# Kernel tuning notes

Hardware: AMD Instinct MI355X
Metric: run time of the kernel (lower is better)

Reference implementation:

```python
import jax, jax.numpy as jnp
import numpy as np

N_NODES = 10000
N_EDGES = 160000
HIDDEN = 64
NUM_RBF = 32
Q_DIM = 8
CUTOFF_UPPER = 5.0


def silu(x):
    return x * jax.nn.sigmoid(x)


def tensor_norm(X):
    # X: [n, 3, 3, H] -> [n, H] (Frobenius norm squared over the 3x3 dims)
    return (X * X).sum(axis=(1, 2))


def decompose_tensor(X):
    # X: [n, 3, 3, H] -> I: [n, H] (trace/3), A: antisym [n,3,3,H], S: sym traceless [n,3,3,H]
    eye = jnp.eye(3, dtype=X.dtype)[None, :, :, None]
    I = jnp.einsum('naah->nh', X) / 3.0
    Xt = X.transpose(0, 2, 1, 3)
    A = 0.5 * (X - Xt)
    S = 0.5 * (X + Xt) - I[:, None, None, :] * eye
    return I, A, S


def compose_tensor(I, A, S):
    eye = jnp.eye(3, dtype=A.dtype)[None, :, :, None]
    return I[:, None, None, :] * eye + A + S


def tmm(P, Q):
    # 3x3 matmul per (atom, channel): [n,3,3,H] x [n,3,3,H] -> [n,3,3,H]
    return jnp.einsum('nach,ncbh->nabh', P, Q)


def setup_inputs() -> dict:
    key = jax.random.key(0)
    ks = jax.random.split(key, 16)
    H = HIDDEN
    inp = {
        'X': jax.random.normal(ks[0], (N_NODES, 3, 3, H), jnp.float32),
        'charges': jax.random.normal(ks[1], (N_NODES, Q_DIM), jnp.float32),
        'edge_weight': jax.random.uniform(ks[2], (N_EDGES,), jnp.float32) * CUTOFF_UPPER,
        'edge_attr': jax.random.normal(ks[3], (N_EDGES, NUM_RBF), jnp.float32),
        'edge_index': jax.random.randint(ks[4], (2, N_EDGES), 0, N_NODES, jnp.int32),
    }
    d_in = NUM_RBF + 2 * Q_DIM
    inp['Ws1'] = jax.random.normal(ks[5], (d_in, H), jnp.float32) / np.sqrt(d_in).astype(np.float32)
    inp['bs1'] = jnp.zeros((H,), jnp.float32)
    inp['Ws2'] = jax.random.normal(ks[6], (H, 2 * H), jnp.float32) / np.sqrt(H).astype(np.float32)
    inp['bs2'] = jnp.zeros((2 * H,), jnp.float32)
    inp['Ws3'] = jax.random.normal(ks[7], (2 * H, 3 * H), jnp.float32) / np.sqrt(2 * H).astype(np.float32)
    inp['bs3'] = jnp.zeros((3 * H,), jnp.float32)
    for i in range(6):
        inp['Wt%d' % i] = jax.random.normal(ks[8 + i], (H, H), jnp.float32) / np.sqrt(H).astype(np.float32)
    return inp


def reference(X, charges, edge_weight, edge_attr, Ws1, bs1, Ws2, bs2, Ws3, bs3,
              Wt0, Wt1, Wt2, Wt3, Wt4, Wt5, edge_index):
    H = HIDDEN
    n = X.shape[0]
    row, col = edge_index[0], edge_index[1]
    # cosine cutoff (cutoff_lower = 0)
    C = 0.5 * (jnp.cos(edge_weight * (jnp.pi / CUTOFF_UPPER)) + 1.0)
    C = C * (edge_weight < CUTOFF_UPPER).astype(X.dtype)
    # edge scalar MLP on [rbf, q_i, q_j]
    h = jnp.concatenate([edge_attr, charges[row], charges[col]], axis=-1)
    h = silu(h @ Ws1 + bs1)
    h = silu(h @ Ws2 + bs2)
    h = silu(h @ Ws3 + bs3)
    w = (h * C[:, None]).reshape(h.shape[0], 3, H)  # [E, 3, H]
    # normalize node tensors
    X = X / (tensor_norm(X) + 1.0)[:, None, None, :]
    I, A, S = decompose_tensor(X)
    I = I @ Wt0
    A = A @ Wt1
    S = S @ Wt2
    Y = compose_tensor(I, A, S)
    # message passing: gather I/A/S at source (edge_index[1]), weight per component, scatter-add at dest (edge_index[0])
    eye = jnp.eye(3, dtype=X.dtype)[None, :, :, None]
    msg_e = ((w[:, 0] * I[col])[:, None, None, :] * eye
             + w[:, 1][:, None, None, :] * A[col]
             + w[:, 2][:, None, None, :] * S[col])  # [E, 3, 3, H]
    msg = jax.ops.segment_sum(msg_e, row, num_segments=n)  # [n, 3, 3, H]
    # O(3): C = msg @ Y + Y @ msg (3x3 matmul per channel)
    Cm = tmm(msg, Y) + tmm(Y, msg)
    I2, A2, S2 = decompose_tensor(Cm)
    normp1 = tensor_norm(Cm) + 1.0
    I2 = I2 / normp1
    A2 = A2 / normp1[:, None, None, :]
    S2 = S2 / normp1[:, None, None, :]
    I2 = I2 @ Wt3
    A2 = A2 @ Wt4
    S2 = S2 @ Wt5
    dX = compose_tensor(I2, A2, S2)
    return X + dX + tmm(dX, dX)
```

## Files before the change

### kernel.cpp

```cpp
#include <hip/hip_runtime.h>
#include <math.h>

#define HD 64

typedef _Float16 half8 __attribute__((ext_vector_type(8)));
typedef _Float16 half4v __attribute__((ext_vector_type(4)));
typedef float floatx4 __attribute__((ext_vector_type(4)));

__device__ __forceinline__ float silu_f(float x) {
    return x * __builtin_amdgcn_rcpf(1.0f + __expf(-x));
}

__global__ __launch_bounds__(256) void node_pre(
    const float* __restrict__ X,
    const float* __restrict__ Wt0, const float* __restrict__ Wt1, const float* __restrict__ Wt2,
    float* __restrict__ Tn, _Float16* __restrict__ TnH, int N)
{
    int sub = threadIdx.x >> 6;
    int h = threadIdx.x & 63;
    int n = blockIdx.x * 4 + sub;
    int nn = (n < N) ? n : (N - 1);

    const float* Xb = X + (size_t)nn * 9 * HD + h;
    float x[9];
    float nrm = 0.f;
#pragma unroll
    for (int i = 0; i < 9; ++i) { x[i] = Xb[i * HD]; nrm += x[i] * x[i]; }
    float inv = 1.0f / (nrm + 1.0f);
#pragma unroll
    for (int i = 0; i < 9; ++i) x[i] *= inv;

    float I0 = (x[0] + x[4] + x[8]) * (1.0f / 3.0f);
    __shared__ float comp[4][10][HD];
    comp[sub][0][h] = I0;
    comp[sub][1][h] = 0.5f * (x[1] - x[3]);
    comp[sub][2][h] = 0.5f * (x[2] - x[6]);
    comp[sub][3][h] = 0.5f * (x[5] - x[7]);
    comp[sub][4][h] = x[0] - I0;
    comp[sub][5][h] = 0.5f * (x[1] + x[3]);
    comp[sub][6][h] = 0.5f * (x[2] + x[6]);
    comp[sub][7][h] = x[4] - I0;
    comp[sub][8][h] = 0.5f * (x[5] + x[7]);
    comp[sub][9][h] = x[8] - I0;
    __syncthreads();
    float acc[10];
#pragma unroll
    for (int i = 0; i < 10; ++i) acc[i] = 0.f;
    for (int k = 0; k < HD; ++k) {
        float w0 = Wt0[k * HD + h];
        float w1 = Wt1[k * HD + h];
        float w2 = Wt2[k * HD + h];
        acc[0] += comp[sub][0][k] * w0;
        acc[1] += comp[sub][1][k] * w1;
        acc[2] += comp[sub][2][k] * w1;
        acc[3] += comp[sub][3][k] * w1;
#pragma unroll
        for (int j = 0; j < 6; ++j) acc[4 + j] += comp[sub][4 + j][k] * w2;
    }
    if (n < N) {
        float* tp = Tn + (size_t)n * 640 + h;
        _Float16* th = TnH + (size_t)n * 640 + h;
#pragma unroll
        for (int i = 0; i < 10; ++i) {
            tp[i * 64] = acc[i];
            th[i * 64] = (_Float16)acc[i];
        }
    }
}

__global__ __launch_bounds__(256) void count_kernel(
    const int* __restrict__ edge_index, int* __restrict__ cnt, int E)
{
    int e = blockIdx.x * 256 + threadIdx.x;
    if (e < E) atomicAdd(&cnt[edge_index[e]], 1);
}

__global__ __launch_bounds__(1024) void scan_kernel(
    const int* __restrict__ cnt, int* __restrict__ offs, int* __restrict__ curs, int N)
{
    __shared__ int partials[16];
    __shared__ int base_s;
    int tid = threadIdx.x, wid = tid >> 6, lane = tid & 63;
    if (tid == 0) base_s = 0;
    __syncthreads();
    for (int start = 0; start < N; start += 1024) {
        int i = start + tid;
        int v = (i < N) ? cnt[i] : 0;
        int s = v;
#pragma unroll
        for (int d = 1; d < 64; d <<= 1) {
            int t = __shfl_up(s, d, 64);
            if (lane >= d) s += t;
        }
        if (lane == 63) partials[wid] = s;
        __syncthreads();
        if (tid == 0) {
            int run = base_s;
#pragma unroll
            for (int w = 0; w < 16; ++w) { int t = partials[w]; partials[w] = run; run += t; }
            base_s = run;
        }
        __syncthreads();
        int excl = partials[wid] + s - v;
        if (i < N) { offs[i] = excl; curs[i] = excl; }
        __syncthreads();
    }
    if (tid == 0) offs[N] = base_s;
}

__global__ __launch_bounds__(256) void place_kernel(
    const int* __restrict__ edge_index, int* __restrict__ curs,
    int* __restrict__ rank, int* __restrict__ colP, int E)
{
    int e = blockIdx.x * 256 + threadIdx.x;
    if (e < E) {
        int p = atomicAdd(&curs[edge_index[e]], 1);
        rank[e] = p;
        colP[p] = edge_index[E + e];
    }
}

__global__ __launch_bounds__(256) void wconv(
    const float* __restrict__ Ws1, const float* __restrict__ Ws2, const float* __restrict__ Ws3,
    _Float16* __restrict__ W1f, _Float16* __restrict__ W2f, _Float16* __restrict__ W3f)
{
    int id = blockIdx.x * 256 + threadIdx.x;
    if (id < 4096) {
        int i = id & 7, l = (id >> 3) & 63, t = id >> 9;
        int s = t >> 2, nt = t & 3;
        int k = s * 32 + (l >> 4) * 8 + i;
        int n = nt * 16 + (l & 15);
        W1f[id] = (k < 48) ? (_Float16)Ws1[k * 64 + n] : (_Float16)0.f;
    } else if (id < 4096 + 8192) {
        int j = id - 4096;
        int i = j & 7, l = (j >> 3) & 63, t = j >> 9;
        int s = t >> 3, nt = t & 7;
        int k = s * 32 + (l >> 4) * 8 + i;
        int n = nt * 16 + (l & 15);
        W2f[j] = (_Float16)Ws2[k * 128 + n];
    } else if (id < 4096 + 8192 + 24576) {
        int j = id - 4096 - 8192;
        int i = j & 7, l = (j >> 3) & 63, t = j >> 9;
        int s = t / 12, nt = t % 12;
        int k = s * 32 + (l >> 4) * 8 + i;
        int n = nt * 16 + (l & 15);
        W3f[j] = (_Float16)Ws3[k * 192 + n];
    }
}

__global__ __launch_bounds__(256, 6) void mlp_mfma(
    const float* __restrict__ edge_attr, const float* __restrict__ charges,
    const float* __restrict__ edge_weight, const int* __restrict__ edge_index,
    const int* __restrict__ rank,
    const _Float16* __restrict__ W1f, const float* __restrict__ bs1,
    const _Float16* __restrict__ W2f, const float* __restrict__ bs2,
    const _Float16* __restrict__ W3f, const float* __restrict__ bs3,
    _Float16* __restrict__ bufH, int E)
{
    __shared__ __align__(16) _Float16 act[4][16][208];
    __shared__ float cvsS[4][16];
    __shared__ int rankSS[4][16];

    int tid = threadIdx.x;
    int wv = tid >> 6, l = tid & 63;
    int base = blockIdx.x * 64 + wv * 16;
    int row16 = l & 15, quad = l >> 4;

#pragma unroll
    for (int i = 0; i < 4; ++i) {
        int slot = l + i * 64;
        int e_l = slot >> 4, f = slot & 15;
        int e = base + e_l;
        int ee = (e < E) ? e : (E - 1);
        float4 v = make_float4(0.f, 0.f, 0.f, 0.f);
        if (f < 8) {
            v = *(const float4*)(edge_attr + (size_t)ee * 32 + f * 4);
        } else if (f < 10) {
            int r = edge_index[ee];
            v = *(const float4*)(charges + (size_t)r * 8 + (f - 8) * 4);
        } else if (f < 12) {
            int c = edge_index[E + ee];
            v = *(const float4*)(charges + (size_t)c * 8 + (f - 10) * 4);
        }
        half4v hv = { (_Float16)v.x, (_Float16)v.y, (_Float16)v.z, (_Float16)v.w };
        *(half4v*)&act[wv][e_l][f * 4] = hv;
    }
    if (l < 16) {
        int e = base + l;
        int ee = (e < E) ? e : (E - 1);
        rankSS[wv][l] = rank[ee];
        float wgt = edge_weight[ee];
        float cv = 0.5f * (__cosf(wgt * 0.6283185307179586f) + 1.0f);
        cvsS[wv][l] = (wgt < 5.0f) ? cv : 0.0f;
    }

    half8 A[4];
    A[0] = *(const half8*)&act[wv][row16][quad * 8];
    A[1] = *(const half8*)&act[wv][row16][32 + quad * 8];
    floatx4 acc1[4];
#pragma unroll
    for (int nt = 0; nt < 4; ++nt) {
        floatx4 c = {0.f, 0.f, 0.f, 0.f};
        c = __builtin_amdgcn_mfma_f32_16x16x32_f16(
                A[0], *(const half8*)(W1f + ((size_t)(0 * 4 + nt) * 64 + l) * 8), c, 0, 0, 0);
        c = __builtin_amdgcn_mfma_f32_16x16x32_f16(
                A[1], *(const half8*)(W1f + ((size_t)(1 * 4 + nt) * 64 + l) * 8), c, 0, 0, 0);
        acc1[nt] = c;
    }
#pragma unroll
    for (int nt = 0; nt < 4; ++nt) {
        float b = bs1[nt * 16 + row16];
#pragma unroll
        for (int r = 0; r < 4; ++r)
            act[wv][quad * 4 + r][64 + nt * 16 + row16] = (_Float16)silu_f(acc1[nt][r] + b);
    }

    A[0] = *(const half8*)&act[wv][row16][64 + quad * 8];
    A[1] = *(const half8*)&act[wv][row16][96 + quad * 8];
    floatx4 acc2[8];
#pragma unroll
    for (int nt = 0; nt < 8; ++nt) {
        floatx4 c = {0.f, 0.f, 0.f, 0.f};
        c = __builtin_amdgcn_mfma_f32_16x16x32_f16(
                A[0], *(const half8*)(W2f + ((size_t)(0 * 8 + nt) * 64 + l) * 8), c, 0, 0, 0);
        c = __builtin_amdgcn_mfma_f32_16x16x32_f16(
                A[1], *(const half8*)(W2f + ((size_t)(1 * 8 + nt) * 64 + l) * 8), c, 0, 0, 0);
        acc2[nt] = c;
    }
#pragma unroll
    for (int nt = 0; nt < 8; ++nt) {
        float b = bs2[nt * 16 + row16];
#pragma unroll
        for (int r = 0; r < 4; ++r)
            act[wv][quad * 4 + r][nt * 16 + row16] = (_Float16)silu_f(acc2[nt][r] + b);
    }

    A[0] = *(const half8*)&act[wv][row16][quad * 8];
    A[1] = *(const half8*)&act[wv][row16][32 + quad * 8];
    A[2] = *(const half8*)&act[wv][row16][64 + quad * 8];
    A[3] = *(const half8*)&act[wv][row16][96 + quad * 8];

    float cvrow[4];
#pragma unroll
    for (int r = 0; r < 4; ++r) cvrow[r] = cvsS[wv][quad * 4 + r];

    floatx4 acc3[12];
#pragma unroll
    for (int nt = 0; nt < 12; ++nt) {
        floatx4 c = {0.f, 0.f, 0.f, 0.f};
#pragma unroll
        for (int s = 0; s < 4; ++s)
            c = __builtin_amdgcn_mfma_f32_16x16x32_f16(
                    A[s], *(const half8*)(W3f + ((size_t)(s * 12 + nt) * 64 + l) * 8), c, 0, 0, 0);
        acc3[nt] = c;
    }
#pragma unroll
    for (int nt = 0; nt < 12; ++nt) {
        float b = bs3[nt * 16 + row16];
#pragma unroll
        for (int r = 0; r < 4; ++r)
            act[wv][quad * 4 + r][nt * 16 + row16] =
                (_Float16)(silu_f(acc3[nt][r] + b) * cvrow[r]);
    }
    {
        int fr = l >> 2;
        int ef = base + fr;
        if (ef < E) {
            _Float16* dst = bufH + (size_t)rankSS[wv][fr] * 192;
#pragma unroll
            for (int i = 0; i < 6; ++i) {
                int j = (l & 3) + i * 4;
                *(half8*)(dst + j * 8) = *(const half8*)&act[wv][fr][j * 8];
            }
        }
    }
}

__global__ __launch_bounds__(256) void msg_kernel(
    const _Float16* __restrict__ bufH, const int* __restrict__ colP,
    const int* __restrict__ offs, const _Float16* __restrict__ TnH,
    float* __restrict__ Mn, int N)
{
    int n = blockIdx.x * 2 + (threadIdx.x >> 7);
    if (n >= N) return;
    int half = (threadIdx.x >> 6) & 1;
    int lane = threadIdx.x & 63;
    int beg = offs[n], end = offs[n + 1];

    if (half == 0) {
        float a0 = 0.f, a1 = 0.f, a2 = 0.f, a3 = 0.f;
#pragma unroll 4
        for (int idx = beg; idx < end; ++idx) {
            int c = colP[idx];
            const _Float16* wp = bufH + (size_t)idx * 192;
            float w0 = (float)wp[lane];
            float w1 = (float)wp[64 + lane];
            const _Float16* tp = TnH + (size_t)c * 640;
            a0 += w0 * (float)tp[lane];
            a1 += w1 * (float)tp[64 + lane];
            a2 += w1 * (float)tp[128 + lane];
            a3 += w1 * (float)tp[192 + lane];
        }
        float* mp = Mn + (size_t)n * 640;
        mp[lane] = a0;
        mp[64 + lane] = a1; mp[128 + lane] = a2; mp[192 + lane] = a3;
    } else {
        float a4 = 0.f, a5 = 0.f, a6 = 0.f, a7 = 0.f, a8 = 0.f, a9 = 0.f;
#pragma unroll 4
        for (int idx = beg; idx < end; ++idx) {
            int c = colP[idx];
            const _Float16* wp = bufH + (size_t)idx * 192;
            float w2 = (float)wp[128 + lane];
            const _Float16* tp = TnH + (size_t)c * 640;
            a4 += w2 * (float)tp[256 + lane];
            a5 += w2 * (float)tp[320 + lane];
            a6 += w2 * (float)tp[384 + lane];
            a7 += w2 * (float)tp[448 + lane];
            a8 += w2 * (float)tp[512 + lane];
            a9 += w2 * (float)tp[576 + lane];
        }
        float* mp = Mn + (size_t)n * 640;
        mp[256 + lane] = a4; mp[320 + lane] = a5; mp[384 + lane] = a6;
        mp[448 + lane] = a7; mp[512 + lane] = a8; mp[576 + lane] = a9;
    }
}

__global__ __launch_bounds__(256) void node_post(
    const float* __restrict__ X,
    const float* __restrict__ Tn, const float* __restrict__ Mn,
    const float* __restrict__ Wt3, const float* __restrict__ Wt4, const float* __restrict__ Wt5,
    float* __restrict__ out, int N)
{
    int sub = threadIdx.x >> 6;
    int h = threadIdx.x & 63;
    int n = blockIdx.x * 4 + sub;
    int nn = (n < N) ? n : (N - 1);

    const float* Xb = X + (size_t)nn * 9 * HD + h;
    float x[9];
    float nr = 0.f;
#pragma unroll
    for (int i = 0; i < 9; ++i) { x[i] = Xb[i * HD]; nr += x[i] * x[i]; }
    float xinv = 1.0f / (nr + 1.0f);
#pragma unroll
    for (int i = 0; i < 9; ++i) x[i] *= xinv;

    const float* tp = Tn + (size_t)nn * 640 + h;
    const float* mp = Mn + (size_t)nn * 640 + h;
    float yI = tp[0], mI = mp[0];
    float yA[3], yS[6], mA[3], mS[6];
#pragma unroll
    for (int j = 0; j < 3; ++j) { yA[j] = tp[(1 + j) * 64]; mA[j] = mp[(1 + j) * 64]; }
#pragma unroll
    for (int j = 0; j < 6; ++j) { yS[j] = tp[(4 + j) * 64]; mS[j] = mp[(4 + j) * 64]; }

    float M[3][3] = {
        { mI + mS[0],     mA[0] + mS[1],   mA[1] + mS[2] },
        { -mA[0] + mS[1], mI + mS[3],      mA[2] + mS[4] },
        { -mA[1] + mS[2], -mA[2] + mS[4],  mI + mS[5] } };
    float Y[3][3] = {
        { yI + yS[0],     yA[0] + yS[1],   yA[1] + yS[2] },
        { -yA[0] + yS[1], yI + yS[3],      yA[2] + yS[4] },
        { -yA[1] + yS[2], -yA[2] + yS[4],  yI + yS[5] } };

    float Cm[3][3];
    float nrm = 0.f;
#pragma unroll
    for (int a = 0; a < 3; ++a) {
#pragma unroll
        for (int b = 0; b < 3; ++b) {
            float s = 0.f;
#pragma unroll
            for (int c = 0; c < 3; ++c) s += M[a][c] * Y[c][b] + Y[a][c] * M[c][b];
            Cm[a][b] = s;
            nrm += s * s;
        }
    }
    float inv = 1.0f / (nrm + 1.0f);
    float tr3 = (Cm[0][0] + Cm[1][1] + Cm[2][2]) * (1.0f / 3.0f);

    __shared__ float comp[4][10][HD];
    comp[sub][0][h] = tr3 * inv;
    comp[sub][1][h] = 0.5f * (Cm[0][1] - Cm[1][0]) * inv;
    comp[sub][2][h] = 0.5f * (Cm[0][2] - Cm[2][0]) * inv;
    comp[sub][3][h] = 0.5f * (Cm[1][2] - Cm[2][1]) * inv;
    comp[sub][4][h] = (Cm[0][0] - tr3) * inv;
    comp[sub][5][h] = 0.5f * (Cm[0][1] + Cm[1][0]) * inv;
    comp[sub][6][h] = 0.5f * (Cm[0][2] + Cm[2][0]) * inv;
    comp[sub][7][h] = (Cm[1][1] - tr3) * inv;
    comp[sub][8][h] = 0.5f * (Cm[1][2] + Cm[2][1]) * inv;
    comp[sub][9][h] = (Cm[2][2] - tr3) * inv;
    __syncthreads();

    float acc[10];
#pragma unroll
    for (int i = 0; i < 10; ++i) acc[i] = 0.f;
    for (int k = 0; k < HD; ++k) {
        float w3 = Wt3[k * HD + h];
        float w4 = Wt4[k * HD + h];
        float w5 = Wt5[k * HD + h];
        acc[0] += comp[sub][0][k] * w3;
        acc[1] += comp[sub][1][k] * w4;
        acc[2] += comp[sub][2][k] * w4;
        acc[3] += comp[sub][3][k] * w4;
#pragma unroll
        for (int j = 0; j < 6; ++j) acc[4 + j] += comp[sub][4 + j][k] * w5;
    }
    float D[3][3] = {
        { acc[0] + acc[4],  acc[1] + acc[5],  acc[2] + acc[6] },
        { -acc[1] + acc[5], acc[0] + acc[7],  acc[3] + acc[8] },
        { -acc[2] + acc[6], -acc[3] + acc[8], acc[0] + acc[9] } };

    if (n < N) {
        float* ob = out + (size_t)n * 9 * HD + h;
#pragma unroll
        for (int a = 0; a < 3; ++a) {
#pragma unroll
            for (int b = 0; b < 3; ++b) {
                float s = 0.f;
#pragma unroll
                for (int c = 0; c < 3; ++c) s += D[a][c] * D[c][b];
                ob[(a * 3 + b) * HD] = x[a * 3 + b] + D[a][b] + s;
            }
        }
    }
}

extern "C" void kernel_launch(void* const* d_in, const int* in_sizes, int n_in,
                              void* d_out, int out_size, void* d_ws, size_t ws_size,
                              hipStream_t stream)
{
    const float* X           = (const float*)d_in[0];
    const float* charges     = (const float*)d_in[1];
    const float* edge_weight = (const float*)d_in[2];
    const float* edge_attr   = (const float*)d_in[3];
    const int*   edge_index  = (const int*)d_in[4];
    const float* Ws1 = (const float*)d_in[5];
    const float* bs1 = (const float*)d_in[6];
    const float* Ws2 = (const float*)d_in[7];
    const float* bs2 = (const float*)d_in[8];
    const float* Ws3 = (const float*)d_in[9];
    const float* bs3 = (const float*)d_in[10];
    const float* Wt0 = (const float*)d_in[11];
    const float* Wt1 = (const float*)d_in[12];
    const float* Wt2 = (const float*)d_in[13];
    const float* Wt3 = (const float*)d_in[14];
    const float* Wt4 = (const float*)d_in[15];
    const float* Wt5 = (const float*)d_in[16];

    int N = in_sizes[0] / (9 * HD);
    int E = in_sizes[2];

    float* ws = (float*)d_ws;
    float* Tn  = ws;
    float* Mn  = Tn + (size_t)N * 640;
    _Float16* TnH  = (_Float16*)(Mn + (size_t)N * 640);
    _Float16* bufH = TnH + (size_t)N * 640;
    int* cnt   = (int*)(bufH + (size_t)E * 192);
    int* offs  = cnt + N;
    int* curs  = offs + N + 1;
    int* rank  = curs + N;
    int* colP  = rank + E;
    size_t fofs = ((size_t)((char*)(colP + E) - (char*)d_ws) + 15) & ~(size_t)15;
    _Float16* W1f = (_Float16*)((char*)d_ws + fofs);
    _Float16* W2f = W1f + 4096;
    _Float16* W3f = W2f + 8192;

    hipMemsetAsync(cnt, 0, (size_t)N * sizeof(int), stream);

    int nbE256 = (E + 255) / 256;
    count_kernel<<<nbE256, 256, 0, stream>>>(edge_index, cnt, E);
    scan_kernel<<<1, 1024, 0, stream>>>(cnt, offs, curs, N);
    place_kernel<<<nbE256, 256, 0, stream>>>(edge_index, curs, rank, colP, E);

    wconv<<<144, 256, 0, stream>>>(Ws1, Ws2, Ws3, W1f, W2f, W3f);

    node_pre<<<(N + 3) / 4, 256, 0, stream>>>(X, Wt0, Wt1, Wt2, Tn, TnH, N);

    int nbE64 = (E + 63) / 64;
    mlp_mfma<<<nbE64, 256, 0, stream>>>(edge_attr, charges, edge_weight, edge_index,
                                        rank, W1f, bs1, W2f, bs2, W3f, bs3, bufH, E);

    msg_kernel<<<(N + 1) / 2, 256, 0, stream>>>(bufH, colP, offs, TnH, Mn, N);

    node_post<<<(N + 3) / 4, 256, 0, stream>>>(X, Tn, Mn, Wt3, Wt4, Wt5, (float*)d_out, N);
}
```

Before: 184.3 us.

## Parallelize CSR scan, split message edges across halves, batch MLP weight loads

The single-block serial scan is replaced by a three-kernel multi-block scan (block scan, partial scan, add-back), which removes a serialized loop over N. The message kernel now splits each node's edge range between two wavefronts that each compute all ten components and combine them through shared memory, so the weight and index reads are no longer duplicated. The MLP kernel preloads weight fragments into registers before issuing its MFMA chains, lowers the launch-bounds occupancy hint from 6 to 4, and shrinks the LDS row padding. The extra kernel launches and the higher register use per wave trade against better memory-level parallelism.

```diff
diff --git a/kernel.cpp b/kernel.cpp
--- a/kernel.cpp
+++ b/kernel.cpp
@@ -75,37 +75,55 @@
     if (e < E) atomicAdd(&cnt[edge_index[e]], 1);
 }
 
-__global__ __launch_bounds__(1024) void scan_kernel(
-    const int* __restrict__ cnt, int* __restrict__ offs, int* __restrict__ curs, int N)
-{
-    __shared__ int partials[16];
-    __shared__ int base_s;
+__global__ __launch_bounds__(1024) void scanA(
+    const int* __restrict__ cnt, int* __restrict__ offs, int* __restrict__ partial, int N)
+{
+    __shared__ int wsum[16];
     int tid = threadIdx.x, wid = tid >> 6, lane = tid & 63;
-    if (tid == 0) base_s = 0;
+    int i = blockIdx.x * 1024 + tid;
+    int v = (i < N) ? cnt[i] : 0;
+    int s = v;
+#pragma unroll
+    for (int d = 1; d < 64; d <<= 1) {
+        int t = __shfl_up(s, d, 64);
+        if (lane >= d) s += t;
+    }
+    if (lane == 63) wsum[wid] = s;
     __syncthreads();
-    for (int start = 0; start < N; start += 1024) {
-        int i = start + tid;
-        int v = (i < N) ? cnt[i] : 0;
-        int s = v;
-#pragma unroll
-        for (int d = 1; d < 64; d <<= 1) {
-            int t = __shfl_up(s, d, 64);
-            if (lane >= d) s += t;
-        }
-        if (lane == 63) partials[wid] = s;
-        __syncthreads();
-        if (tid == 0) {
-            int run = base_s;
-#pragma unroll
-            for (int w = 0; w < 16; ++w) { int t = partials[w]; partials[w] = run; run += t; }
-            base_s = run;
-        }
-        __syncthreads();
-        int excl = partials[wid] + s - v;
-        if (i < N) { offs[i] = excl; curs[i] = excl; }
-        __syncthreads();
-    }
-    if (tid == 0) offs[N] = base_s;
+    if (tid == 0) {
+        int run = 0;
+#pragma unroll
+        for (int w = 0; w < 16; ++w) { int t = wsum[w]; wsum[w] = run; run += t; }
+        partial[blockIdx.x] = run;
+    }
+    __syncthreads();
+    if (i < N) offs[i] = wsum[wid] + s - v;
+}
+
+__global__ __launch_bounds__(64) void scanB(int* __restrict__ partial, int nb)
+{
+    int lane = threadIdx.x;
+    int v = (lane < nb) ? partial[lane] : 0;
+    int s = v;
+#pragma unroll
+    for (int d = 1; d < 64; d <<= 1) {
+        int t = __shfl_up(s, d, 64);
+        if (lane >= d) s += t;
+    }
+    if (lane < nb) partial[lane] = s - v;
+}
+
+__global__ __launch_bounds__(256) void scanC(
+    int* __restrict__ offs, const int* __restrict__ partial, int* __restrict__ curs,
+    int N, int E)
+{
+    int i = blockIdx.x * 256 + threadIdx.x;
+    if (i < N) {
+        int o = offs[i] + partial[i >> 10];
+        offs[i] = o;
+        curs[i] = o;
+    }
+    if (i == 0) offs[N] = E;
 }
 
 __global__ __launch_bounds__(256) void place_kernel(
@@ -148,7 +166,7 @@
     }
 }
 
-__global__ __launch_bounds__(256, 6) void mlp_mfma(
+__global__ __launch_bounds__(256, 4) void mlp_mfma(
     const float* __restrict__ edge_attr, const float* __restrict__ charges,
     const float* __restrict__ edge_weight, const int* __restrict__ edge_index,
     const int* __restrict__ rank,
@@ -157,7 +175,7 @@
     const _Float16* __restrict__ W3f, const float* __restrict__ bs3,
     _Float16* __restrict__ bufH, int E)
 {
-    __shared__ __align__(16) _Float16 act[4][16][208];
+    __shared__ __align__(16) _Float16 act[4][16][200];
     __shared__ float cvsS[4][16];
     __shared__ int rankSS[4][16];
 
@@ -198,14 +216,18 @@
     A[0] = *(const half8*)&act[wv][row16][quad * 8];
     A[1] = *(const half8*)&act[wv][row16][32 + quad * 8];
     floatx4 acc1[4];
-#pragma unroll
-    for (int nt = 0; nt < 4; ++nt) {
-        floatx4 c = {0.f, 0.f, 0.f, 0.f};
-        c = __builtin_amdgcn_mfma_f32_16x16x32_f16(
-                A[0], *(const half8*)(W1f + ((size_t)(0 * 4 + nt) * 64 + l) * 8), c, 0, 0, 0);
-        c = __builtin_amdgcn_mfma_f32_16x16x32_f16(
-                A[1], *(const half8*)(W1f + ((size_t)(1 * 4 + nt) * 64 + l) * 8), c, 0, 0, 0);
-        acc1[nt] = c;
+    {
+        half8 W[8];
+#pragma unroll
+        for (int t = 0; t < 8; ++t)
+            W[t] = *(const half8*)(W1f + ((size_t)t * 64 + l) * 8);
+#pragma unroll
+        for (int nt = 0; nt < 4; ++nt) {
+            floatx4 c = {0.f, 0.f, 0.f, 0.f};
+            c = __builtin_amdgcn_mfma_f32_16x16x32_f16(A[0], W[nt], c, 0, 0, 0);
+            c = __builtin_amdgcn_mfma_f32_16x16x32_f16(A[1], W[4 + nt], c, 0, 0, 0);
+            acc1[nt] = c;
+        }
     }
 #pragma unroll
     for (int nt = 0; nt < 4; ++nt) {
@@ -219,13 +241,16 @@
     A[1] = *(const half8*)&act[wv][row16][96 + quad * 8];
     floatx4 acc2[8];
 #pragma unroll
-    for (int nt = 0; nt < 8; ++nt) {
-        floatx4 c = {0.f, 0.f, 0.f, 0.f};
-        c = __builtin_amdgcn_mfma_f32_16x16x32_f16(
-                A[0], *(const half8*)(W2f + ((size_t)(0 * 8 + nt) * 64 + l) * 8), c, 0, 0, 0);
-        c = __builtin_amdgcn_mfma_f32_16x16x32_f16(
-                A[1], *(const half8*)(W2f + ((size_t)(1 * 8 + nt) * 64 + l) * 8), c, 0, 0, 0);
-        acc2[nt] = c;
+    for (int nt = 0; nt < 8; ++nt) acc2[nt] = (floatx4){0.f, 0.f, 0.f, 0.f};
+#pragma unroll
+    for (int s = 0; s < 2; ++s) {
+        half8 W[8];
+#pragma unroll
+        for (int nt = 0; nt < 8; ++nt)
+            W[nt] = *(const half8*)(W2f + ((size_t)(s * 8 + nt) * 64 + l) * 8);
+#pragma unroll
+        for (int nt = 0; nt < 8; ++nt)
+            acc2[nt] = __builtin_amdgcn_mfma_f32_16x16x32_f16(A[s], W[nt], acc2[nt], 0, 0, 0);
     }
 #pragma unroll
     for (int nt = 0; nt < 8; ++nt) {
@@ -244,23 +269,30 @@
 #pragma unroll
     for (int r = 0; r < 4; ++r) cvrow[r] = cvsS[wv][quad * 4 + r];
 
-    floatx4 acc3[12];
-#pragma unroll
-    for (int nt = 0; nt < 12; ++nt) {
-        floatx4 c = {0.f, 0.f, 0.f, 0.f};
-#pragma unroll
-        for (int s = 0; s < 4; ++s)
-            c = __builtin_amdgcn_mfma_f32_16x16x32_f16(
-                    A[s], *(const half8*)(W3f + ((size_t)(s * 12 + nt) * 64 + l) * 8), c, 0, 0, 0);
-        acc3[nt] = c;
-    }
-#pragma unroll
-    for (int nt = 0; nt < 12; ++nt) {
-        float b = bs3[nt * 16 + row16];
-#pragma unroll
-        for (int r = 0; r < 4; ++r)
-            act[wv][quad * 4 + r][nt * 16 + row16] =
-                (_Float16)(silu_f(acc3[nt][r] + b) * cvrow[r]);
+#pragma unroll
+    for (int g = 0; g < 2; ++g) {
+        floatx4 acc3[6];
+#pragma unroll
+        for (int j = 0; j < 6; ++j) acc3[j] = (floatx4){0.f, 0.f, 0.f, 0.f};
+#pragma unroll
+        for (int s = 0; s < 4; ++s) {
+            half8 W[6];
+#pragma unroll
+            for (int j = 0; j < 6; ++j)
+                W[j] = *(const half8*)(W3f + ((size_t)(s * 12 + g * 6 + j) * 64 + l) * 8);
+#pragma unroll
+            for (int j = 0; j < 6; ++j)
+                acc3[j] = __builtin_amdgcn_mfma_f32_16x16x32_f16(A[s], W[j], acc3[j], 0, 0, 0);
+        }
+#pragma unroll
+        for (int j = 0; j < 6; ++j) {
+            int nt = g * 6 + j;
+            float b = bs3[nt * 16 + row16];
+#pragma unroll
+            for (int r = 0; r < 4; ++r)
+                act[wv][quad * 4 + r][nt * 16 + row16] =
+                    (_Float16)(silu_f(acc3[j][r] + b) * cvrow[r]);
+        }
     }
     {
         int fr = l >> 2;
@@ -281,47 +313,52 @@
     const int* __restrict__ offs, const _Float16* __restrict__ TnH,
     float* __restrict__ Mn, int N)
 {
-    int n = blockIdx.x * 2 + (threadIdx.x >> 7);
-    if (n >= N) return;
+    __shared__ float part[2][2][10][64];
+    int slot = threadIdx.x >> 7;
     int half = (threadIdx.x >> 6) & 1;
     int lane = threadIdx.x & 63;
-    int beg = offs[n], end = offs[n + 1];
-
-    if (half == 0) {
-        float a0 = 0.f, a1 = 0.f, a2 = 0.f, a3 = 0.f;
-#pragma unroll 4
-        for (int idx = beg; idx < end; ++idx) {
-            int c = colP[idx];
-            const _Float16* wp = bufH + (size_t)idx * 192;
-            float w0 = (float)wp[lane];
-            float w1 = (float)wp[64 + lane];
-            const _Float16* tp = TnH + (size_t)c * 640;
-            a0 += w0 * (float)tp[lane];
-            a1 += w1 * (float)tp[64 + lane];
-            a2 += w1 * (float)tp[128 + lane];
-            a3 += w1 * (float)tp[192 + lane];
-        }
+    int n = blockIdx.x * 2 + slot;
+    int nn = (n < N) ? n : (N - 1);
+    int beg = offs[nn], end = offs[nn + 1];
+    int mid = beg + ((end - beg + 1) >> 1);
+    int s0 = half ? mid : beg;
+    int s1 = half ? end : mid;
+
+    float a0 = 0.f, a1 = 0.f, a2 = 0.f, a3 = 0.f, a4 = 0.f;
+    float a5 = 0.f, a6 = 0.f, a7 = 0.f, a8 = 0.f, a9 = 0.f;
+#pragma unroll 2
+    for (int idx = s0; idx < s1; ++idx) {
+        int c = colP[idx];
+        const _Float16* wp = bufH + (size_t)idx * 192;
+        float w0 = (float)wp[lane];
+        float w1 = (float)wp[64 + lane];
+        float w2 = (float)wp[128 + lane];
+        const _Float16* tp = TnH + (size_t)c * 640;
+        a0 += w0 * (float)tp[lane];
+        a1 += w1 * (float)tp[64 + lane];
+        a2 += w1 * (float)tp[128 + lane];
+        a3 += w1 * (float)tp[192 + lane];
+        a4 += w2 * (float)tp[256 + lane];
+        a5 += w2 * (float)tp[320 + lane];
+        a6 += w2 * (float)tp[384 + lane];
+        a7 += w2 * (float)tp[448 + lane];
+        a8 += w2 * (float)tp[512 + lane];
+        a9 += w2 * (float)tp[576 + lane];
+    }
+    part[slot][half][0][lane] = a0; part[slot][half][1][lane] = a1;
+    part[slot][half][2][lane] = a2; part[slot][half][3][lane] = a3;
+    part[slot][half][4][lane] = a4; part[slot][half][5][lane] = a5;
+    part[slot][half][6][lane] = a6; part[slot][half][7][lane] = a7;
+    part[slot][half][8][lane] = a8; part[slot][half][9][lane] = a9;
+    __syncthreads();
+
+    if (n < N) {
         float* mp = Mn + (size_t)n * 640;
-        mp[lane] = a0;
-        mp[64 + lane] = a1; mp[128 + lane] = a2; mp[192 + lane] = a3;
-    } else {
-        float a4 = 0.f, a5 = 0.f, a6 = 0.f, a7 = 0.f, a8 = 0.f, a9 = 0.f;
-#pragma unroll 4
-        for (int idx = beg; idx < end; ++idx) {
-            int c = colP[idx];
-            const _Float16* wp = bufH + (size_t)idx * 192;
-            float w2 = (float)wp[128 + lane];
-            const _Float16* tp = TnH + (size_t)c * 640;
-            a4 += w2 * (float)tp[256 + lane];
-            a5 += w2 * (float)tp[320 + lane];
-            a6 += w2 * (float)tp[384 + lane];
-            a7 += w2 * (float)tp[448 + lane];
-            a8 += w2 * (float)tp[512 + lane];
-            a9 += w2 * (float)tp[576 + lane];
-        }
-        float* mp = Mn + (size_t)n * 640;
-        mp[256 + lane] = a4; mp[320 + lane] = a5; mp[384 + lane] = a6;
-        mp[448 + lane] = a7; mp[512 + lane] = a8; mp[576 + lane] = a9;
+#pragma unroll
+        for (int j = 0; j < 5; ++j) {
+            int c = half * 5 + j;
+            mp[c * 64 + lane] = part[slot][0][c][lane] + part[slot][1][c][lane];
+        }
     }
 }
 
@@ -461,7 +498,8 @@
     int* curs  = offs + N + 1;
     int* rank  = curs + N;
     int* colP  = rank + E;
-    size_t fofs = ((size_t)((char*)(colP + E) - (char*)d_ws) + 15) & ~(size_t)15;
+    int* partial = colP + E;
+    size_t fofs = ((size_t)((char*)(partial + 64) - (char*)d_ws) + 15) & ~(size_t)15;
     _Float16* W1f = (_Float16*)((char*)d_ws + fofs);
     _Float16* W2f = W1f + 4096;
     _Float16* W3f = W2f + 8192;
@@ -469,8 +507,11 @@
     hipMemsetAsync(cnt, 0, (size_t)N * sizeof(int), stream);
 
     int nbE256 = (E + 255) / 256;
+    int nbN1024 = (N + 1023) / 1024;
     count_kernel<<<nbE256, 256, 0, stream>>>(edge_index, cnt, E);
-    scan_kernel<<<1, 1024, 0, stream>>>(cnt, offs, curs, N);
+    scanA<<<nbN1024, 1024, 0, stream>>>(cnt, offs, partial, N);
+    scanB<<<1, 64, 0, stream>>>(partial, nbN1024);
+    scanC<<<(N + 255) / 256, 256, 0, stream>>>(offs, partial, curs, N, E);
     place_kernel<<<nbE256, 256, 0, stream>>>(edge_index, curs, rank, colP, E);
 
     wconv<<<144, 256, 0, stream>>>(Ws1, Ws2, Ws3, W1f, W2f, W3f);
```

Result: faster. 178.8 us (-3.0%).
